# Kernel optimization log

Hardware: AMD Instinct MI355X
Metric: run time of the kernel (lower is better)

The kernel has to match this reference:

```python
import jax, jax.numpy as jnp
import numpy as np
from jax import lax

B, N, C, H = 32, 1025, 512, 8
HD = C // H            # head dim = 64
HS = WS = 32           # feature map size, N = 1 + HS*WS
SCALE = HD ** -0.5
SPLITS = (128, 192, 192)  # window {3:2,5:3,7:3} * head_dim


def setup_inputs() -> dict:
    key = jax.random.key(0)
    ks = jax.random.split(key, 11)
    return {
        "x": jax.random.normal(ks[0], (B, N, C), jnp.float32),
        "Wqkv": jax.random.normal(ks[1], (C, 3 * C), jnp.float32) * 0.02,
        "bqkv": jnp.zeros((3 * C,), jnp.float32),
        "Wproj": jax.random.normal(ks[2], (C, C), jnp.float32) * 0.02,
        "bproj": jnp.zeros((C,), jnp.float32),
        "ck3": jax.random.normal(ks[3], (3, 3, 1, SPLITS[0]), jnp.float32) * 0.1,
        "cb3": jnp.zeros((SPLITS[0],), jnp.float32),
        "ck5": jax.random.normal(ks[4], (5, 5, 1, SPLITS[1]), jnp.float32) * 0.1,
        "cb5": jnp.zeros((SPLITS[1],), jnp.float32),
        "ck7": jax.random.normal(ks[5], (7, 7, 1, SPLITS[2]), jnp.float32) * 0.1,
        "cb7": jnp.zeros((SPLITS[2],), jnp.float32),
    }


def _dwconv(x, kern, bias):
    # depthwise conv, Keras Conv2D(groups=C, filters=C, padding='same')
    out = lax.conv_general_dilated(
        x, kern, window_strides=(1, 1), padding="SAME",
        dimension_numbers=("NHWC", "HWIO", "NHWC"),
        feature_group_count=x.shape[-1])
    return out + bias


def reference(x, Wqkv, bqkv, Wproj, bproj, ck3, cb3, ck5, cb5, ck7, cb7):
    # qkv projection: [B,N,3C] -> [B,N,3,H,HD]
    qkv = (x @ Wqkv + bqkv).reshape(B, N, 3, H, HD)
    q, k, v = qkv[:, :, 0], qkv[:, :, 1], qkv[:, :, 2]

    # factorized linear attention: softmax over token axis N
    k_softmax = jax.nn.softmax(k, axis=1)
    ksv = jnp.einsum("bnhk,bnhv->bhkv", k_softmax, v)      # [B,H,HD,HD]
    factor_att = jnp.einsum("bnhk,bhkv->bnhv", q, ksv)     # [B,N,H,HD]

    # conv relative position encoding on image tokens
    v_img = v[:, 1:].reshape(B, HS, WS, C)
    v2, v3, v4 = jnp.split(v_img, np.cumsum(SPLITS)[:-1].tolist(), axis=3)
    conv_v = jnp.concatenate(
        [_dwconv(v2, ck3, cb3), _dwconv(v3, ck5, cb5), _dwconv(v4, ck7, cb7)],
        axis=3).reshape(B, HS * WS, H, HD)
    ev_img = q[:, 1:] * conv_v
    crpe = jnp.concatenate(
        [jnp.zeros((B, 1, H, HD), x.dtype), ev_img], axis=1)  # [B,N,H,HD]

    out = (SCALE * factor_att + crpe).reshape(B, N, C)
    return out @ Wproj + bproj
```

## Files before the change

### kernel.cpp

```cpp
#include <hip/hip_runtime.h>
#include <hip/hip_bf16.h>

#define BB 32
#define NN 1025
#define CC 512
#define HH 8
#define HD 64
#define MM (BB * NN)
#define MP 33024
#define KK 512
#define SCALE 0.125f

typedef unsigned short u16;
typedef __attribute__((ext_vector_type(4))) unsigned short u16x4;
typedef __attribute__((ext_vector_type(8))) unsigned short u16x8;
typedef __attribute__((ext_vector_type(4))) float f32x4;
typedef __attribute__((ext_vector_type(8))) __bf16 bf16x8;

__device__ __forceinline__ u16 f2bf(float f) {
    unsigned u = __float_as_uint(f);
    unsigned r = (u + 0x7FFFu + ((u >> 16) & 1u)) >> 16;
    return (u16)r;
}
__device__ __forceinline__ float bf2f(u16 h) {
    return __uint_as_float((unsigned)h << 16);
}

__device__ __forceinline__ void gload16(const u16* g, u16* l) {
    __builtin_amdgcn_global_load_lds(
        (const __attribute__((address_space(1))) unsigned int*)g,
        (__attribute__((address_space(3))) unsigned int*)l, 16, 0, 0);
}

__global__ __launch_bounds__(256) void convert_x_kernel(
    const float* __restrict__ x, u16* __restrict__ xbf)
{
    size_t t = (size_t)blockIdx.x * 256 + threadIdx.x;
    size_t base = t * 8;
    u16x8 o;
    if (base < (size_t)MM * CC) {
        f32x4 a = *(const f32x4*)&x[base];
        f32x4 b = *(const f32x4*)&x[base + 4];
#pragma unroll
        for (int j = 0; j < 4; j++) { o[j] = f2bf(a[j]); o[j + 4] = f2bf(b[j]); }
    } else {
#pragma unroll
        for (int j = 0; j < 8; j++) o[j] = 0;
    }
    *(u16x8*)&xbf[base] = o;
}

__global__ __launch_bounds__(256) void convert_wt_kernel(
    const float* __restrict__ W, u16* __restrict__ Wt, int N)
{
    int t = blockIdx.x * 256 + threadIdx.x;
    int n = t >> 6;
    int k0 = (t & 63) * 8;
    u16x8 o;
#pragma unroll
    for (int j = 0; j < 8; j++) o[j] = f2bf(W[(size_t)(k0 + j) * N + n]);
    *(u16x8*)&Wt[(size_t)n * KK + k0] = o;
}

__global__ __launch_bounds__(256) void prep_w7_kernel(
    const float* __restrict__ ck3, const float* __restrict__ cb3,
    const float* __restrict__ ck5, const float* __restrict__ cb5,
    const float* __restrict__ ck7, const float* __restrict__ cb7,
    float* __restrict__ w7, float* __restrict__ cbx)
{
    int t = blockIdx.x * 256 + threadIdx.x;
    if (t >= 49 * 512) return;
    int c = t & 511;
    int tap = t >> 9;
    int dy = tap / 7, dx = tap % 7;
    float w = 0.f;
    if (c < 128) {
        int ry = dy - 2, rx = dx - 2;
        if (ry >= 0 && ry < 3 && rx >= 0 && rx < 3) w = ck3[(ry * 3 + rx) * 128 + c];
    } else if (c < 320) {
        int ry = dy - 1, rx = dx - 1;
        if (ry >= 0 && ry < 5 && rx >= 0 && rx < 5) w = ck5[(ry * 5 + rx) * 192 + (c - 128)];
    } else {
        w = ck7[(dy * 7 + dx) * 192 + (c - 320)];
    }
    w7[tap * 512 + c] = w;
    if (t < 512)
        cbx[t] = (t < 128) ? cb3[t] : (t < 320) ? cb5[t - 128] : cb7[t - 320];
}

template <int MODE, int NSZ, int GX>
__global__ __launch_bounds__(256) void gemm_bf16_kernel(
    const u16* __restrict__ A, const u16* __restrict__ Bt,
    const float* __restrict__ bias, void* __restrict__ outv, int nwg)
{
    __shared__ __align__(16) u16 lds[2][2][4096];

    int wg = blockIdx.x;
    {
        int q = nwg >> 3, r = nwg & 7;
        int xcd = wg & 7, pos = wg >> 3;
        wg = (xcd < r ? xcd * (q + 1) : r * (q + 1) + (xcd - r) * q) + pos;
    }
    const int m0 = (wg / GX) * 128;
    const int n0 = (wg % GX) * 128;

    const int t = threadIdx.x;

    const int srow = t >> 2;
    const int ps   = t & 3;
    const int ls   = ps ^ ((srow >> 1) & 3);
    const u16* gA = A  + (size_t)(m0 + srow) * KK + ls * 8;
    const u16* gB = Bt + (size_t)(n0 + srow) * KK + ls * 8;

    const int l  = t & 63;
    const int w  = t >> 6;
    const int wm = (w >> 1) * 64;
    const int wn = (w & 1) * 64;
    const int lr = l & 15;
    const int s  = l >> 4;
    const int ra = wm + lr;
    const int rb = wn + lr;
    const int offA = ra * 32 + (s ^ ((ra >> 1) & 3)) * 8;
    const int offB = rb * 32 + (s ^ ((rb >> 1) & 3)) * 8;

    f32x4 acc[4][4] = {};

#define STAGE(buf, kk_) do {                                        \
        gload16(gA + (kk_),           &lds[buf][0][t * 8]);         \
        gload16(gA + 64 * KK + (kk_), &lds[buf][0][2048 + t * 8]);  \
        gload16(gB + (kk_),           &lds[buf][1][t * 8]);         \
        gload16(gB + 64 * KK + (kk_), &lds[buf][1][2048 + t * 8]);  \
    } while (0)

    STAGE(0, 0);
    __syncthreads();

    int cur = 0;
    for (int step = 0; step < 16; ++step) {
        if (step < 15) STAGE(cur ^ 1, (step + 1) * 32);
        bf16x8 a[4], b[4];
#pragma unroll
        for (int i = 0; i < 4; i++) a[i] = *(const bf16x8*)&lds[cur][0][offA + i * 512];
#pragma unroll
        for (int i = 0; i < 4; i++) b[i] = *(const bf16x8*)&lds[cur][1][offB + i * 512];
#pragma unroll
        for (int i = 0; i < 4; i++)
#pragma unroll
            for (int j = 0; j < 4; j++)
                acc[i][j] = __builtin_amdgcn_mfma_f32_16x16x32_bf16(a[i], b[j], acc[i][j], 0, 0, 0);
        __syncthreads();
        cur ^= 1;
    }
#undef STAGE

    const int row0 = m0 + wm + (l >> 4) * 4;
    const int col0 = n0 + wn + lr;
    float bs[4];
#pragma unroll
    for (int j = 0; j < 4; j++) bs[j] = bias[col0 + j * 16];

    if (MODE == 0) {
        u16* qkv = (u16*)outv;
        const int plane = n0 >> 9;
        u16* pl = qkv + (size_t)plane * ((size_t)MP * CC);
#pragma unroll
        for (int i = 0; i < 4; i++) {
#pragma unroll
            for (int j = 0; j < 4; j++) {
                int gc = (col0 + j * 16) & 511;
#pragma unroll
                for (int r = 0; r < 4; r++) {
                    int gm = row0 + i * 16 + r;
                    pl[(size_t)gm * CC + gc] = f2bf(acc[i][j][r] + bs[j]);
                }
            }
        }
    } else {
        float* out = (float*)outv;
#pragma unroll
        for (int i = 0; i < 4; i++) {
#pragma unroll
            for (int j = 0; j < 4; j++) {
                int gn = col0 + j * 16;
#pragma unroll
                for (int r = 0; r < 4; r++) {
                    int gm = row0 + i * 16 + r;
                    if (gm < MM) out[(size_t)gm * NSZ + gn] = acc[i][j][r] + bs[j];
                }
            }
        }
    }
}

__global__ __launch_bounds__(256) void ksv_part_kernel(
    const u16* __restrict__ kbf, const u16* __restrict__ vbf,
    float* __restrict__ part, float* __restrict__ psum)
{
    int bh = blockIdx.x;
    int chunk = blockIdx.y;
    int b = bh >> 3, h = bh & 7;
    int n0 = chunk * 256;
    int n1 = (chunk == 3) ? NN : n0 + 256;

    __shared__ float ke[16][64];
    __shared__ float ve[16][64];

    int t = threadIdx.x;
    int lrow = t >> 4;
    int lcol = (t & 15) * 4;
    int tx = t & 15, ty = t >> 4;

    float acc[4][4] = {};
    float cs[4] = {};
    for (int nb = n0; nb < n1; nb += 16) {
        int n = nb + lrow;
        bool valid = n < n1;
        size_t off = ((size_t)(b * NN + n)) * CC + h * HD + lcol;
        u16x4 kr = *(const u16x4*)&kbf[off];
        u16x4 vr = *(const u16x4*)&vbf[off];
#pragma unroll
        for (int j = 0; j < 4; j++) {
            ke[lrow][lcol + j] = valid ? __expf(bf2f(kr[j])) : 0.f;
            ve[lrow][lcol + j] = valid ? bf2f(vr[j]) : 0.f;
        }
        __syncthreads();
#pragma unroll 4
        for (int d = 0; d < 16; d++) {
            f32x4 ka = *(const f32x4*)&ke[d][ty * 4];
            f32x4 vb = *(const f32x4*)&ve[d][tx * 4];
#pragma unroll
            for (int i = 0; i < 4; i++)
#pragma unroll
                for (int j = 0; j < 4; j++)
                    acc[i][j] = fmaf(ka[i], vb[j], acc[i][j]);
        }
        if (t < 16) {
#pragma unroll
            for (int d = 0; d < 16; d++) {
                f32x4 kv = *(const f32x4*)&ke[d][t * 4];
#pragma unroll
                for (int j = 0; j < 4; j++) cs[j] += kv[j];
            }
        }
        __syncthreads();
    }

    float* dst = part + ((size_t)chunk * 256 + bh) * 4096;
#pragma unroll
    for (int i = 0; i < 4; i++) {
        f32x4 o = {acc[i][0], acc[i][1], acc[i][2], acc[i][3]};
        *(f32x4*)&dst[(ty * 4 + i) * 64 + tx * 4] = o;
    }
    if (t < 16) {
        f32x4 o = {cs[0], cs[1], cs[2], cs[3]};
        *(f32x4*)&psum[((size_t)chunk * 256 + bh) * 64 + t * 4] = o;
    }
}

__global__ __launch_bounds__(256) void ksv_reduceT_kernel(
    const float* __restrict__ part, const float* __restrict__ psum,
    u16* __restrict__ ksvT)
{
    int i = blockIdx.x * 256 + threadIdx.x;
    size_t e = (size_t)i * 4;
    int bh = (int)(e >> 12);
    int kk = ((int)e >> 6) & 63;
    int vv0 = (int)e & 63;
    f32x4 s = *(const f32x4*)&part[e];
    float cs = psum[bh * 64 + kk];
#pragma unroll
    for (int c = 1; c < 4; c++) {
        f32x4 p = *(const f32x4*)&part[(size_t)c * 256 * 4096 + e];
#pragma unroll
        for (int j = 0; j < 4; j++) s[j] += p[j];
        cs += psum[(size_t)c * 256 * 64 + bh * 64 + kk];
    }
    float inv = SCALE / cs;
#pragma unroll
    for (int j = 0; j < 4; j++)
        ksvT[(size_t)bh * 4096 + (vv0 + j) * 64 + kk] = f2bf(s[j] * inv);
}

__global__ __launch_bounds__(256) void attn_ev_kernel(
    const u16* __restrict__ qbf, const u16* __restrict__ vbf,
    const u16* __restrict__ ksvT, const float* __restrict__ w7,
    const float* __restrict__ cbx, u16* __restrict__ attbf)
{
    int yg = blockIdx.x;
    int bh = blockIdx.y;
    int b = bh >> 3, h = bh & 7;
    const int nbase = 1 + yg * 128;

    __shared__ __align__(16) u16 lq[128 * 64];
    __shared__ __align__(16) u16 lk[64 * 64];
    __shared__ __align__(16) u16 lv[10 * 32 * 64];
    __shared__ __align__(16) u16 latt[128 * 64];

    int t = threadIdx.x;

#pragma unroll
    for (int i = 0; i < 4; i++) {
        int idx = t + i * 256;
        int row = idx >> 3, sl = idx & 7;
        u16x8 v = *(const u16x8*)&qbf[((size_t)(b * NN + nbase + row)) * CC + h * HD + sl * 8];
        *(u16x8*)&lq[row * 64 + ((sl ^ (row & 7)) * 8)] = v;
    }
#pragma unroll
    for (int i = 0; i < 2; i++) {
        int idx = t + i * 256;
        int col = idx >> 3, sl = idx & 7;
        u16x8 v = *(const u16x8*)&ksvT[(size_t)bh * 4096 + col * 64 + sl * 8];
        *(u16x8*)&lk[col * 64 + ((col & 7) ^ sl) * 8] = v;
    }
    {
        int x = t >> 3, sl = t & 7;
#pragma unroll
        for (int s = 0; s < 10; s++) {
            int yy = yg * 4 - 3 + s;
            u16x8 v;
            if (yy >= 0 && yy < 32)
                v = *(const u16x8*)&vbf[((size_t)(b * NN) + 1 + yy * 32 + x) * CC + h * HD + sl * 8];
            else {
#pragma unroll
                for (int j = 0; j < 8; j++) v[j] = 0;
            }
            *(u16x8*)&lv[s * 2048 + x * 64 + sl * 8] = v;
        }
    }
    __syncthreads();

    {
        int l = t & 63, w = t >> 6;
        int lr = l & 15, ls = l >> 4;
        f32x4 acc[2][4] = {};
#pragma unroll
        for (int kf = 0; kf < 2; kf++) {
            bf16x8 a[2], bf[4];
#pragma unroll
            for (int i = 0; i < 2; i++) {
                int row = w * 32 + i * 16 + lr;
                a[i] = *(const bf16x8*)&lq[row * 64 + (((kf * 4 + ls) ^ (row & 7)) * 8)];
            }
#pragma unroll
            for (int j = 0; j < 4; j++) {
                int col = j * 16 + lr;
                bf[j] = *(const bf16x8*)&lk[col * 64 + (((kf * 4 + ls) ^ (col & 7)) * 8)];
            }
#pragma unroll
            for (int i = 0; i < 2; i++)
#pragma unroll
                for (int j = 0; j < 4; j++)
                    acc[i][j] = __builtin_amdgcn_mfma_f32_16x16x32_bf16(a[i], bf[j], acc[i][j], 0, 0, 0);
        }
#pragma unroll
        for (int i = 0; i < 2; i++)
#pragma unroll
            for (int j = 0; j < 4; j++)
#pragma unroll
                for (int r = 0; r < 4; r++)
                    latt[(w * 32 + i * 16 + ls * 4 + r) * 64 + j * 16 + lr] =
                        f2bf(acc[i][j][r]);
    }
    __syncthreads();

    int oct = t >> 4;
    int cq = t & 15;
    int c4 = cq * 4;
    int c = h * HD + c4;
    int yo = oct >> 2;
    int x0 = (oct & 3) * 8;

    float a2[8][4];
    {
        f32x4 b0 = *(const f32x4*)&cbx[c];
#pragma unroll
        for (int xi = 0; xi < 8; xi++)
#pragma unroll
            for (int j = 0; j < 4; j++) a2[xi][j] = b0[j];
    }

    for (int dy = 0; dy < 7; dy++) {
        int s = yo + dy;
        float wr[7][4];
#pragma unroll
        for (int dx = 0; dx < 7; dx++)
            *(f32x4*)&wr[dx][0] = *(const f32x4*)&w7[(dy * 7 + dx) * 512 + c];
        u16x4 vv[14];
#pragma unroll
        for (int sxi = 0; sxi < 14; sxi++) {
            int sx = x0 - 3 + sxi;
            int sxc = sx < 0 ? 0 : (sx > 31 ? 31 : sx);
            vv[sxi] = *(const u16x4*)&lv[s * 2048 + sxc * 64 + c4];
        }
#pragma unroll
        for (int sxi = 0; sxi < 14; sxi++) {
            int sx = x0 - 3 + sxi;
            bool xval = (sx >= 0) && (sx < 32);
            float vf[4];
#pragma unroll
            for (int j = 0; j < 4; j++) vf[j] = xval ? bf2f(vv[sxi][j]) : 0.f;
            int lo = sxi - 6 > 0 ? sxi - 6 : 0;
            int hi = sxi < 7 ? sxi : 7;
#pragma unroll
            for (int xi = 0; xi < 8; xi++) {
                if (xi < lo || xi > hi) continue;
                int dx = sxi - xi;
#pragma unroll
                for (int j = 0; j < 4; j++)
                    a2[xi][j] = fmaf(vf[j], wr[dx][j], a2[xi][j]);
            }
        }
    }

#pragma unroll
    for (int xi = 0; xi < 8; xi++) {
        int row = oct * 8 + xi;
        u16x4 at = *(const u16x4*)&latt[row * 64 + c4];
        u16x4 qv = *(const u16x4*)&lq[row * 64 + (((cq >> 1) ^ (row & 7)) * 8) + (cq & 1) * 4];
        u16x4 ov;
#pragma unroll
        for (int j = 0; j < 4; j++)
            ov[j] = f2bf(bf2f(at[j]) + bf2f(qv[j]) * a2[xi][j]);
        *(u16x4*)&attbf[((size_t)(b * NN + nbase + row)) * CC + c] = ov;
    }
}

__global__ __launch_bounds__(512) void att0_kernel(
    const u16* __restrict__ qbf, const u16* __restrict__ ksvT,
    u16* __restrict__ attbf)
{
    int b = blockIdx.x;
    int c = threadIdx.x;
    int h = c >> 6, vv = c & 63;
    const u16* q0 = qbf + (size_t)(b * NN) * CC + h * HD;
    const u16* kb = ksvT + ((size_t)(b * 8 + h)) * 4096 + vv * 64;
    float s = 0.f;
#pragma unroll 8
    for (int kk = 0; kk < 64; kk++)
        s = fmaf(bf2f(q0[kk]), bf2f(kb[kk]), s);
    attbf[(size_t)(b * NN) * CC + c] = f2bf(s);
}

extern "C" void kernel_launch(void* const* d_in, const int* in_sizes, int n_in,
                              void* d_out, int out_size, void* d_ws, size_t ws_size,
                              hipStream_t stream)
{
    const float* x     = (const float*)d_in[0];
    const float* Wqkv  = (const float*)d_in[1];
    const float* bqkv  = (const float*)d_in[2];
    const float* Wproj = (const float*)d_in[3];
    const float* bproj = (const float*)d_in[4];
    const float* ck3   = (const float*)d_in[5];
    const float* cb3   = (const float*)d_in[6];
    const float* ck5   = (const float*)d_in[7];
    const float* cb5   = (const float*)d_in[8];
    const float* ck7   = (const float*)d_in[9];
    const float* cb7   = (const float*)d_in[10];
    float* out = (float*)d_out;

    const size_t PLANE = (size_t)MP * CC;

    u16* xbf  = (u16*)d_ws;
    u16* qbf  = xbf + PLANE;
    u16* kbf  = qbf + PLANE;
    u16* vbf  = kbf + PLANE;
    u16* wqT  = vbf + PLANE;
    u16* wpT  = wqT + (size_t)1536 * 512;
    u16* ksvT = wpT + (size_t)512 * 512;
    float* psum = (float*)(ksvT + (size_t)256 * 4096);
    float* part = psum + (size_t)4 * 256 * 64;
    float* w7   = part + (size_t)4 * 256 * 4096;
    float* cbx  = w7 + 49 * 512;
    u16* attbf = xbf;

    convert_x_kernel<<<(int)(PLANE / 8 / 256), 256, 0, stream>>>(x, xbf);
    convert_wt_kernel<<<1536 * 64 / 256, 256, 0, stream>>>(Wqkv, wqT, 1536);
    convert_wt_kernel<<<512 * 64 / 256, 256, 0, stream>>>(Wproj, wpT, 512);
    prep_w7_kernel<<<98, 256, 0, stream>>>(ck3, cb3, ck5, cb5, ck7, cb7, w7, cbx);

    {
        int nwg = 12 * (MP / 128);
        gemm_bf16_kernel<0, 1536, 12><<<nwg, 256, 0, stream>>>(xbf, wqT, bqkv, qbf, nwg);
    }
    {
        dim3 grid(BB * HH, 4);
        ksv_part_kernel<<<grid, 256, 0, stream>>>(kbf, vbf, part, psum);
        ksv_reduceT_kernel<<<256 * 4096 / 4 / 256, 256, 0, stream>>>(part, psum, ksvT);
    }
    {
        dim3 grid(8, BB * HH);
        attn_ev_kernel<<<grid, 256, 0, stream>>>(qbf, vbf, ksvT, w7, cbx, attbf);
        att0_kernel<<<BB, 512, 0, stream>>>(qbf, ksvT, attbf);
    }
    {
        int nwg = 4 * (MP / 128);
        gemm_bf16_kernel<1, 512, 4><<<nwg, 256, 0, stream>>>(attbf, wpT, bproj, out, nwg);
    }
}
```

Before: 237.6 us.

## Fuse fp32-to-bf16 conversion of x into QKV GEMM and merge small launches

Drops the separate pass that converts x to bf16. The QKV GEMM now loads fp32 rows of x directly into registers, packs them with v_cvt_pk_bf16_f32 and writes them to LDS, while the weight tiles still use global_load_lds. The weight-transpose and conv-weight prep kernels are merged into one launch, and the class-token attention row is folded into the attn_ev grid as an extra block column. This removes a full read and write of x and two launches. In exchange the GEMM A-operand path goes through registers, reading twice the bytes per tile and adding conversion work inside the main loop.

```diff
diff --git a/kernel.cpp b/kernel.cpp
--- a/kernel.cpp
+++ b/kernel.cpp
@@ -32,66 +32,62 @@
         (__attribute__((address_space(3))) unsigned int*)l, 16, 0, 0);
 }
 
-__global__ __launch_bounds__(256) void convert_x_kernel(
-    const float* __restrict__ x, u16* __restrict__ xbf)
-{
-    size_t t = (size_t)blockIdx.x * 256 + threadIdx.x;
-    size_t base = t * 8;
-    u16x8 o;
-    if (base < (size_t)MM * CC) {
-        f32x4 a = *(const f32x4*)&x[base];
-        f32x4 b = *(const f32x4*)&x[base + 4];
-#pragma unroll
-        for (int j = 0; j < 4; j++) { o[j] = f2bf(a[j]); o[j + 4] = f2bf(b[j]); }
-    } else {
-#pragma unroll
-        for (int j = 0; j < 8; j++) o[j] = 0;
-    }
-    *(u16x8*)&xbf[base] = o;
-}
-
-__global__ __launch_bounds__(256) void convert_wt_kernel(
-    const float* __restrict__ W, u16* __restrict__ Wt, int N)
-{
-    int t = blockIdx.x * 256 + threadIdx.x;
-    int n = t >> 6;
-    int k0 = (t & 63) * 8;
-    u16x8 o;
-#pragma unroll
-    for (int j = 0; j < 8; j++) o[j] = f2bf(W[(size_t)(k0 + j) * N + n]);
-    *(u16x8*)&Wt[(size_t)n * KK + k0] = o;
-}
-
-__global__ __launch_bounds__(256) void prep_w7_kernel(
+__device__ __forceinline__ u16x8 cvt8(f32x4 a, f32x4 b) {
+    union { unsigned u[4]; u16x8 v; } r;
+    asm("v_cvt_pk_bf16_f32 %0, %1, %2" : "=v"(r.u[0]) : "v"(a[0]), "v"(a[1]));
+    asm("v_cvt_pk_bf16_f32 %0, %1, %2" : "=v"(r.u[1]) : "v"(a[2]), "v"(a[3]));
+    asm("v_cvt_pk_bf16_f32 %0, %1, %2" : "=v"(r.u[2]) : "v"(b[0]), "v"(b[1]));
+    asm("v_cvt_pk_bf16_f32 %0, %1, %2" : "=v"(r.u[3]) : "v"(b[2]), "v"(b[3]));
+    return r.v;
+}
+
+__global__ __launch_bounds__(256) void prep_all_kernel(
+    const float* __restrict__ Wqkv, const float* __restrict__ Wproj,
     const float* __restrict__ ck3, const float* __restrict__ cb3,
     const float* __restrict__ ck5, const float* __restrict__ cb5,
     const float* __restrict__ ck7, const float* __restrict__ cb7,
+    u16* __restrict__ wqT, u16* __restrict__ wpT,
     float* __restrict__ w7, float* __restrict__ cbx)
 {
-    int t = blockIdx.x * 256 + threadIdx.x;
-    if (t >= 49 * 512) return;
-    int c = t & 511;
-    int tap = t >> 9;
-    int dy = tap / 7, dx = tap % 7;
-    float w = 0.f;
-    if (c < 128) {
-        int ry = dy - 2, rx = dx - 2;
-        if (ry >= 0 && ry < 3 && rx >= 0 && rx < 3) w = ck3[(ry * 3 + rx) * 128 + c];
-    } else if (c < 320) {
-        int ry = dy - 1, rx = dx - 1;
-        if (ry >= 0 && ry < 5 && rx >= 0 && rx < 5) w = ck5[(ry * 5 + rx) * 192 + (c - 128)];
+    int blk = blockIdx.x;
+    int tid = threadIdx.x;
+    if (blk < 512) {
+        const float* W = (blk < 384) ? Wqkv : Wproj;
+        u16* Wt = (blk < 384) ? wqT : wpT;
+        int N = (blk < 384) ? 1536 : 512;
+        int t = (blk < 384 ? blk : blk - 384) * 256 + tid;
+        int n = t >> 6;
+        int k0 = (t & 63) * 8;
+        u16x8 o;
+#pragma unroll
+        for (int j = 0; j < 8; j++) o[j] = f2bf(W[(size_t)(k0 + j) * N + n]);
+        *(u16x8*)&Wt[(size_t)n * KK + k0] = o;
     } else {
-        w = ck7[(dy * 7 + dx) * 192 + (c - 320)];
-    }
-    w7[tap * 512 + c] = w;
-    if (t < 512)
-        cbx[t] = (t < 128) ? cb3[t] : (t < 320) ? cb5[t - 128] : cb7[t - 320];
-}
-
-template <int MODE, int NSZ, int GX>
-__global__ __launch_bounds__(256) void gemm_bf16_kernel(
-    const u16* __restrict__ A, const u16* __restrict__ Bt,
-    const float* __restrict__ bias, void* __restrict__ outv, int nwg)
+        int t = (blk - 512) * 256 + tid;
+        if (t >= 49 * 512) return;
+        int c = t & 511;
+        int tap = t >> 9;
+        int dy = tap / 7, dx = tap % 7;
+        float w = 0.f;
+        if (c < 128) {
+            int ry = dy - 2, rx = dx - 2;
+            if (ry >= 0 && ry < 3 && rx >= 0 && rx < 3) w = ck3[(ry * 3 + rx) * 128 + c];
+        } else if (c < 320) {
+            int ry = dy - 1, rx = dx - 1;
+            if (ry >= 0 && ry < 5 && rx >= 0 && rx < 5) w = ck5[(ry * 5 + rx) * 192 + (c - 128)];
+        } else {
+            w = ck7[(dy * 7 + dx) * 192 + (c - 320)];
+        }
+        w7[tap * 512 + c] = w;
+        if (t < 512)
+            cbx[t] = (t < 128) ? cb3[t] : (t < 320) ? cb5[t - 128] : cb7[t - 320];
+    }
+}
+
+template <int GX>
+__global__ __launch_bounds__(256) void gemm_qkv_kernel(
+    const float* __restrict__ X, const u16* __restrict__ Bt,
+    const float* __restrict__ bias, u16* __restrict__ qkv, int nwg)
 {
     __shared__ __align__(16) u16 lds[2][2][4096];
 
@@ -109,7 +105,10 @@
     const int srow = t >> 2;
     const int ps   = t & 3;
     const int ls   = ps ^ ((srow >> 1) & 3);
-    const u16* gA = A  + (size_t)(m0 + srow) * KK + ls * 8;
+    int ar0 = m0 + srow;      if (ar0 >= MM) ar0 = MM - 1;
+    int ar1 = m0 + 64 + srow; if (ar1 >= MM) ar1 = MM - 1;
+    const float* gA0 = X + (size_t)ar0 * KK + ls * 8;
+    const float* gA1 = X + (size_t)ar1 * KK + ls * 8;
     const u16* gB = Bt + (size_t)(n0 + srow) * KK + ls * 8;
 
     const int l  = t & 63;
@@ -125,6 +124,104 @@
 
     f32x4 acc[4][4] = {};
 
+    {
+        f32x4 p00 = *(const f32x4*)&gA0[0], p01 = *(const f32x4*)&gA0[4];
+        f32x4 p10 = *(const f32x4*)&gA1[0], p11 = *(const f32x4*)&gA1[4];
+        gload16(gB, &lds[0][1][t * 8]);
+        gload16(gB + 64 * KK, &lds[0][1][2048 + t * 8]);
+        *(u16x8*)&lds[0][0][t * 8] = cvt8(p00, p01);
+        *(u16x8*)&lds[0][0][2048 + t * 8] = cvt8(p10, p11);
+    }
+    __syncthreads();
+
+    int cur = 0;
+    for (int step = 0; step < 16; ++step) {
+        int nxt = cur ^ 1;
+        f32x4 p00, p01, p10, p11;
+        if (step < 15) {
+            int kn = (step + 1) * 32;
+            p00 = *(const f32x4*)&gA0[kn];     p01 = *(const f32x4*)&gA0[kn + 4];
+            p10 = *(const f32x4*)&gA1[kn];     p11 = *(const f32x4*)&gA1[kn + 4];
+            gload16(gB + kn, &lds[nxt][1][t * 8]);
+            gload16(gB + 64 * KK + kn, &lds[nxt][1][2048 + t * 8]);
+        }
+        bf16x8 a[4], b[4];
+#pragma unroll
+        for (int i = 0; i < 4; i++) a[i] = *(const bf16x8*)&lds[cur][0][offA + i * 512];
+#pragma unroll
+        for (int i = 0; i < 4; i++) b[i] = *(const bf16x8*)&lds[cur][1][offB + i * 512];
+#pragma unroll
+        for (int i = 0; i < 4; i++)
+#pragma unroll
+            for (int j = 0; j < 4; j++)
+                acc[i][j] = __builtin_amdgcn_mfma_f32_16x16x32_bf16(a[i], b[j], acc[i][j], 0, 0, 0);
+        if (step < 15) {
+            *(u16x8*)&lds[nxt][0][t * 8] = cvt8(p00, p01);
+            *(u16x8*)&lds[nxt][0][2048 + t * 8] = cvt8(p10, p11);
+        }
+        __syncthreads();
+        cur = nxt;
+    }
+
+    const int row0 = m0 + wm + (l >> 4) * 4;
+    const int col0 = n0 + wn + lr;
+    float bs[4];
+#pragma unroll
+    for (int j = 0; j < 4; j++) bs[j] = bias[col0 + j * 16];
+
+    const int plane = n0 >> 9;
+    u16* pl = qkv + (size_t)plane * ((size_t)MP * CC);
+#pragma unroll
+    for (int i = 0; i < 4; i++) {
+#pragma unroll
+        for (int j = 0; j < 4; j++) {
+            int gc = (col0 + j * 16) & 511;
+#pragma unroll
+            for (int r = 0; r < 4; r++) {
+                int gm = row0 + i * 16 + r;
+                pl[(size_t)gm * CC + gc] = f2bf(acc[i][j][r] + bs[j]);
+            }
+        }
+    }
+}
+
+template <int NSZ, int GX>
+__global__ __launch_bounds__(256) void gemm_proj_kernel(
+    const u16* __restrict__ A, const u16* __restrict__ Bt,
+    const float* __restrict__ bias, float* __restrict__ out, int nwg)
+{
+    __shared__ __align__(16) u16 lds[2][2][4096];
+
+    int wg = blockIdx.x;
+    {
+        int q = nwg >> 3, r = nwg & 7;
+        int xcd = wg & 7, pos = wg >> 3;
+        wg = (xcd < r ? xcd * (q + 1) : r * (q + 1) + (xcd - r) * q) + pos;
+    }
+    const int m0 = (wg / GX) * 128;
+    const int n0 = (wg % GX) * 128;
+
+    const int t = threadIdx.x;
+
+    const int srow = t >> 2;
+    const int ps   = t & 3;
+    const int ls   = ps ^ ((srow >> 1) & 3);
+    const u16* gA = A  + (size_t)(m0 + srow) * KK + ls * 8;
+    const u16* gB = Bt + (size_t)(n0 + srow) * KK + ls * 8;
+
+    const int l  = t & 63;
+    const int w  = t >> 6;
+    const int wm = (w >> 1) * 64;
+    const int wn = (w & 1) * 64;
+    const int lr = l & 15;
+    const int s  = l >> 4;
+    const int ra = wm + lr;
+    const int rb = wn + lr;
+    const int offA = ra * 32 + (s ^ ((ra >> 1) & 3)) * 8;
+    const int offB = rb * 32 + (s ^ ((rb >> 1) & 3)) * 8;
+
+    f32x4 acc[4][4] = {};
+
 #define STAGE(buf, kk_) do {                                        \
         gload16(gA + (kk_),           &lds[buf][0][t * 8]);         \
         gload16(gA + 64 * KK + (kk_), &lds[buf][0][2048 + t * 8]);  \
@@ -159,34 +256,15 @@
 #pragma unroll
     for (int j = 0; j < 4; j++) bs[j] = bias[col0 + j * 16];
 
-    if (MODE == 0) {
-        u16* qkv = (u16*)outv;
-        const int plane = n0 >> 9;
-        u16* pl = qkv + (size_t)plane * ((size_t)MP * CC);
-#pragma unroll
-        for (int i = 0; i < 4; i++) {
-#pragma unroll
-            for (int j = 0; j < 4; j++) {
-                int gc = (col0 + j * 16) & 511;
-#pragma unroll
-                for (int r = 0; r < 4; r++) {
-                    int gm = row0 + i * 16 + r;
-                    pl[(size_t)gm * CC + gc] = f2bf(acc[i][j][r] + bs[j]);
-                }
-            }
-        }
-    } else {
-        float* out = (float*)outv;
-#pragma unroll
-        for (int i = 0; i < 4; i++) {
-#pragma unroll
-            for (int j = 0; j < 4; j++) {
-                int gn = col0 + j * 16;
-#pragma unroll
-                for (int r = 0; r < 4; r++) {
-                    int gm = row0 + i * 16 + r;
-                    if (gm < MM) out[(size_t)gm * NSZ + gn] = acc[i][j][r] + bs[j];
-                }
+#pragma unroll
+    for (int i = 0; i < 4; i++) {
+#pragma unroll
+        for (int j = 0; j < 4; j++) {
+            int gn = col0 + j * 16;
+#pragma unroll
+            for (int r = 0; r < 4; r++) {
+                int gm = row0 + i * 16 + r;
+                if (gm < MM) out[(size_t)gm * NSZ + gn] = acc[i][j][r] + bs[j];
             }
         }
     }
@@ -289,14 +367,27 @@
     int yg = blockIdx.x;
     int bh = blockIdx.y;
     int b = bh >> 3, h = bh & 7;
+    int t = threadIdx.x;
+
+    if (yg == 8) {
+        if (t < 64) {
+            const u16* q0 = qbf + (size_t)(b * NN) * CC + h * HD;
+            const u16* kb = ksvT + (size_t)bh * 4096 + t * 64;
+            float s = 0.f;
+#pragma unroll 8
+            for (int kk = 0; kk < 64; kk++)
+                s = fmaf(bf2f(q0[kk]), bf2f(kb[kk]), s);
+            attbf[(size_t)(b * NN) * CC + h * HD + t] = f2bf(s);
+        }
+        return;
+    }
+
     const int nbase = 1 + yg * 128;
 
     __shared__ __align__(16) u16 lq[128 * 64];
     __shared__ __align__(16) u16 lk[64 * 64];
     __shared__ __align__(16) u16 lv[10 * 32 * 64];
     __shared__ __align__(16) u16 latt[128 * 64];
-
-    int t = threadIdx.x;
 
 #pragma unroll
     for (int i = 0; i < 4; i++) {
@@ -423,22 +514,6 @@
             ov[j] = f2bf(bf2f(at[j]) + bf2f(qv[j]) * a2[xi][j]);
         *(u16x4*)&attbf[((size_t)(b * NN + nbase + row)) * CC + c] = ov;
     }
-}
-
-__global__ __launch_bounds__(512) void att0_kernel(
-    const u16* __restrict__ qbf, const u16* __restrict__ ksvT,
-    u16* __restrict__ attbf)
-{
-    int b = blockIdx.x;
-    int c = threadIdx.x;
-    int h = c >> 6, vv = c & 63;
-    const u16* q0 = qbf + (size_t)(b * NN) * CC + h * HD;
-    const u16* kb = ksvT + ((size_t)(b * 8 + h)) * 4096 + vv * 64;
-    float s = 0.f;
-#pragma unroll 8
-    for (int kk = 0; kk < 64; kk++)
-        s = fmaf(bf2f(q0[kk]), bf2f(kb[kk]), s);
-    attbf[(size_t)(b * NN) * CC + c] = f2bf(s);
 }
 
 extern "C" void kernel_launch(void* const* d_in, const int* in_sizes, int n_in,
@@ -460,27 +535,24 @@
 
     const size_t PLANE = (size_t)MP * CC;
 
-    u16* xbf  = (u16*)d_ws;
-    u16* qbf  = xbf + PLANE;
-    u16* kbf  = qbf + PLANE;
-    u16* vbf  = kbf + PLANE;
-    u16* wqT  = vbf + PLANE;
-    u16* wpT  = wqT + (size_t)1536 * 512;
-    u16* ksvT = wpT + (size_t)512 * 512;
+    u16* qbf   = (u16*)d_ws;
+    u16* kbf   = qbf + PLANE;
+    u16* vbf   = kbf + PLANE;
+    u16* attbf = vbf + PLANE;
+    u16* wqT   = attbf + PLANE;
+    u16* wpT   = wqT + (size_t)1536 * 512;
+    u16* ksvT  = wpT + (size_t)512 * 512;
     float* psum = (float*)(ksvT + (size_t)256 * 4096);
     float* part = psum + (size_t)4 * 256 * 64;
     float* w7   = part + (size_t)4 * 256 * 4096;
     float* cbx  = w7 + 49 * 512;
-    u16* attbf = xbf;
-
-    convert_x_kernel<<<(int)(PLANE / 8 / 256), 256, 0, stream>>>(x, xbf);
-    convert_wt_kernel<<<1536 * 64 / 256, 256, 0, stream>>>(Wqkv, wqT, 1536);
-    convert_wt_kernel<<<512 * 64 / 256, 256, 0, stream>>>(Wproj, wpT, 512);
-    prep_w7_kernel<<<98, 256, 0, stream>>>(ck3, cb3, ck5, cb5, ck7, cb7, w7, cbx);
+
+    prep_all_kernel<<<610, 256, 0, stream>>>(
+        Wqkv, Wproj, ck3, cb3, ck5, cb5, ck7, cb7, wqT, wpT, w7, cbx);
 
     {
         int nwg = 12 * (MP / 128);
-        gemm_bf16_kernel<0, 1536, 12><<<nwg, 256, 0, stream>>>(xbf, wqT, bqkv, qbf, nwg);
+        gemm_qkv_kernel<12><<<nwg, 256, 0, stream>>>(x, wqT, bqkv, qbf, nwg);
     }
     {
         dim3 grid(BB * HH, 4);
@@ -488,12 +560,11 @@
         ksv_reduceT_kernel<<<256 * 4096 / 4 / 256, 256, 0, stream>>>(part, psum, ksvT);
     }
     {
-        dim3 grid(8, BB * HH);
+        dim3 grid(9, BB * HH);
         attn_ev_kernel<<<grid, 256, 0, stream>>>(qbf, vbf, ksvT, w7, cbx, attbf);
-        att0_kernel<<<BB, 512, 0, stream>>>(qbf, ksvT, attbf);
     }
     {
         int nwg = 4 * (MP / 128);
-        gemm_bf16_kernel<1, 512, 4><<<nwg, 256, 0, stream>>>(attbf, wpT, bproj, out, nwg);
-    }
-}
+        gemm_proj_kernel<512, 4><<<nwg, 256, 0, stream>>>(attbf, wpT, bproj, out, nwg);
+    }
+}
```

New measurement: 253.1 us. 6.5% more time.

## Stage QKV GEMM epilogue through LDS and merge small prep/att0 launches

Applied to the files above, without the earlier changes.

The QKV GEMM epilogue now writes bf16 results into a swizzled LDS tile and then stores 16-byte vectors row by row, replacing scattered 2-byte global stores. The weight-transpose and conv-weight prep kernels are merged into one launch, and the CLS-token att0 computation is folded into the attn_ev kernel as an extra grid column. This cuts the number of kernel launches and aims for coalesced QKV writes, at the cost of an extra LDS round trip and a barrier in the epilogue.

```diff
diff --git a/kernel.cpp b/kernel.cpp
--- a/kernel.cpp
+++ b/kernel.cpp
@@ -50,42 +50,47 @@
     *(u16x8*)&xbf[base] = o;
 }
 
-__global__ __launch_bounds__(256) void convert_wt_kernel(
-    const float* __restrict__ W, u16* __restrict__ Wt, int N)
-{
-    int t = blockIdx.x * 256 + threadIdx.x;
-    int n = t >> 6;
-    int k0 = (t & 63) * 8;
-    u16x8 o;
-#pragma unroll
-    for (int j = 0; j < 8; j++) o[j] = f2bf(W[(size_t)(k0 + j) * N + n]);
-    *(u16x8*)&Wt[(size_t)n * KK + k0] = o;
-}
-
-__global__ __launch_bounds__(256) void prep_w7_kernel(
+__global__ __launch_bounds__(256) void prep_all_kernel(
+    const float* __restrict__ Wqkv, const float* __restrict__ Wproj,
     const float* __restrict__ ck3, const float* __restrict__ cb3,
     const float* __restrict__ ck5, const float* __restrict__ cb5,
     const float* __restrict__ ck7, const float* __restrict__ cb7,
+    u16* __restrict__ wqT, u16* __restrict__ wpT,
     float* __restrict__ w7, float* __restrict__ cbx)
 {
-    int t = blockIdx.x * 256 + threadIdx.x;
-    if (t >= 49 * 512) return;
-    int c = t & 511;
-    int tap = t >> 9;
-    int dy = tap / 7, dx = tap % 7;
-    float w = 0.f;
-    if (c < 128) {
-        int ry = dy - 2, rx = dx - 2;
-        if (ry >= 0 && ry < 3 && rx >= 0 && rx < 3) w = ck3[(ry * 3 + rx) * 128 + c];
-    } else if (c < 320) {
-        int ry = dy - 1, rx = dx - 1;
-        if (ry >= 0 && ry < 5 && rx >= 0 && rx < 5) w = ck5[(ry * 5 + rx) * 192 + (c - 128)];
+    int blk = blockIdx.x;
+    int tid = threadIdx.x;
+    if (blk < 512) {
+        const float* W = (blk < 384) ? Wqkv : Wproj;
+        u16* Wt = (blk < 384) ? wqT : wpT;
+        int N = (blk < 384) ? 1536 : 512;
+        int t = (blk < 384 ? blk : blk - 384) * 256 + tid;
+        int n = t >> 6;
+        int k0 = (t & 63) * 8;
+        u16x8 o;
+#pragma unroll
+        for (int j = 0; j < 8; j++) o[j] = f2bf(W[(size_t)(k0 + j) * N + n]);
+        *(u16x8*)&Wt[(size_t)n * KK + k0] = o;
     } else {
-        w = ck7[(dy * 7 + dx) * 192 + (c - 320)];
-    }
-    w7[tap * 512 + c] = w;
-    if (t < 512)
-        cbx[t] = (t < 128) ? cb3[t] : (t < 320) ? cb5[t - 128] : cb7[t - 320];
+        int t = (blk - 512) * 256 + tid;
+        if (t >= 49 * 512) return;
+        int c = t & 511;
+        int tap = t >> 9;
+        int dy = tap / 7, dx = tap % 7;
+        float w = 0.f;
+        if (c < 128) {
+            int ry = dy - 2, rx = dx - 2;
+            if (ry >= 0 && ry < 3 && rx >= 0 && rx < 3) w = ck3[(ry * 3 + rx) * 128 + c];
+        } else if (c < 320) {
+            int ry = dy - 1, rx = dx - 1;
+            if (ry >= 0 && ry < 5 && rx >= 0 && rx < 5) w = ck5[(ry * 5 + rx) * 192 + (c - 128)];
+        } else {
+            w = ck7[(dy * 7 + dx) * 192 + (c - 320)];
+        }
+        w7[tap * 512 + c] = w;
+        if (t < 512)
+            cbx[t] = (t < 128) ? cb3[t] : (t < 320) ? cb5[t - 128] : cb7[t - 320];
+    }
 }
 
 template <int MODE, int NSZ, int GX>
@@ -153,30 +158,41 @@
     }
 #undef STAGE
 
-    const int row0 = m0 + wm + (l >> 4) * 4;
     const int col0 = n0 + wn + lr;
     float bs[4];
 #pragma unroll
     for (int j = 0; j < 4; j++) bs[j] = bias[col0 + j * 16];
 
     if (MODE == 0) {
-        u16* qkv = (u16*)outv;
+        u16* eb = &lds[0][0][0];
+        const int rl0 = wm + (l >> 4) * 4;
+        const int cl0 = wn + lr;
+#pragma unroll
+        for (int i = 0; i < 4; i++) {
+#pragma unroll
+            for (int j = 0; j < 4; j++) {
+#pragma unroll
+                for (int r = 0; r < 4; r++) {
+                    int row = rl0 + i * 16 + r;
+                    int a_ = (row * 256 + (cl0 + j * 16) * 2) ^ ((row & 12) << 3);
+                    eb[a_ >> 1] = f2bf(acc[i][j][r] + bs[j]);
+                }
+            }
+        }
+        __syncthreads();
         const int plane = n0 >> 9;
-        u16* pl = qkv + (size_t)plane * ((size_t)MP * CC);
-#pragma unroll
-        for (int i = 0; i < 4; i++) {
-#pragma unroll
-            for (int j = 0; j < 4; j++) {
-                int gc = (col0 + j * 16) & 511;
-#pragma unroll
-                for (int r = 0; r < 4; r++) {
-                    int gm = row0 + i * 16 + r;
-                    pl[(size_t)gm * CC + gc] = f2bf(acc[i][j][r] + bs[j]);
-                }
-            }
+        u16* pl = (u16*)outv + (size_t)plane * ((size_t)MP * CC) + (n0 & 511);
+#pragma unroll
+        for (int s2 = 0; s2 < 8; s2++) {
+            int flat = s2 * 2048 + t * 8;
+            int row = flat >> 7, col = flat & 127;
+            int a_ = (row * 256 + col * 2) ^ ((row & 12) << 3);
+            u16x8 v = *(const u16x8*)((const char*)eb + a_);
+            *(u16x8*)&pl[(size_t)(m0 + row) * CC + col] = v;
         }
     } else {
         float* out = (float*)outv;
+        const int row0 = m0 + wm + (l >> 4) * 4;
 #pragma unroll
         for (int i = 0; i < 4; i++) {
 #pragma unroll
@@ -289,14 +305,27 @@
     int yg = blockIdx.x;
     int bh = blockIdx.y;
     int b = bh >> 3, h = bh & 7;
+    int t = threadIdx.x;
+
+    if (yg == 8) {
+        if (t < 64) {
+            const u16* q0 = qbf + (size_t)(b * NN) * CC + h * HD;
+            const u16* kb = ksvT + (size_t)bh * 4096 + t * 64;
+            float s = 0.f;
+#pragma unroll 8
+            for (int kk = 0; kk < 64; kk++)
+                s = fmaf(bf2f(q0[kk]), bf2f(kb[kk]), s);
+            attbf[(size_t)(b * NN) * CC + h * HD + t] = f2bf(s);
+        }
+        return;
+    }
+
     const int nbase = 1 + yg * 128;
 
     __shared__ __align__(16) u16 lq[128 * 64];
     __shared__ __align__(16) u16 lk[64 * 64];
     __shared__ __align__(16) u16 lv[10 * 32 * 64];
     __shared__ __align__(16) u16 latt[128 * 64];
-
-    int t = threadIdx.x;
 
 #pragma unroll
     for (int i = 0; i < 4; i++) {
@@ -423,22 +452,6 @@
             ov[j] = f2bf(bf2f(at[j]) + bf2f(qv[j]) * a2[xi][j]);
         *(u16x4*)&attbf[((size_t)(b * NN + nbase + row)) * CC + c] = ov;
     }
-}
-
-__global__ __launch_bounds__(512) void att0_kernel(
-    const u16* __restrict__ qbf, const u16* __restrict__ ksvT,
-    u16* __restrict__ attbf)
-{
-    int b = blockIdx.x;
-    int c = threadIdx.x;
-    int h = c >> 6, vv = c & 63;
-    const u16* q0 = qbf + (size_t)(b * NN) * CC + h * HD;
-    const u16* kb = ksvT + ((size_t)(b * 8 + h)) * 4096 + vv * 64;
-    float s = 0.f;
-#pragma unroll 8
-    for (int kk = 0; kk < 64; kk++)
-        s = fmaf(bf2f(q0[kk]), bf2f(kb[kk]), s);
-    attbf[(size_t)(b * NN) * CC + c] = f2bf(s);
 }
 
 extern "C" void kernel_launch(void* const* d_in, const int* in_sizes, int n_in,
@@ -473,10 +486,9 @@
     float* cbx  = w7 + 49 * 512;
     u16* attbf = xbf;
 
+    prep_all_kernel<<<610, 256, 0, stream>>>(
+        Wqkv, Wproj, ck3, cb3, ck5, cb5, ck7, cb7, wqT, wpT, w7, cbx);
     convert_x_kernel<<<(int)(PLANE / 8 / 256), 256, 0, stream>>>(x, xbf);
-    convert_wt_kernel<<<1536 * 64 / 256, 256, 0, stream>>>(Wqkv, wqT, 1536);
-    convert_wt_kernel<<<512 * 64 / 256, 256, 0, stream>>>(Wproj, wpT, 512);
-    prep_w7_kernel<<<98, 256, 0, stream>>>(ck3, cb3, ck5, cb5, ck7, cb7, w7, cbx);
 
     {
         int nwg = 12 * (MP / 128);
@@ -488,9 +500,8 @@
         ksv_reduceT_kernel<<<256 * 4096 / 4 / 256, 256, 0, stream>>>(part, psum, ksvT);
     }
     {
-        dim3 grid(8, BB * HH);
+        dim3 grid(9, BB * HH);
         attn_ev_kernel<<<grid, 256, 0, stream>>>(qbf, vbf, ksvT, w7, cbx, attbf);
-        att0_kernel<<<BB, 512, 0, stream>>>(qbf, ksvT, attbf);
     }
     {
         int nwg = 4 * (MP / 128);
```

New measurement: 231.4 us. 1.03x faster.
